# Kernel optimization log

Measured on AMD Instinct MI355X. Metric: run time of the kernel, lower is better.

## Reference

```python
import jax, jax.numpy as jnp
import numpy as np

# Module hyperparameters
P_, K_, NH = 8, 4, 8
B, H, W, C = 2, 64, 24, 256


def setup_inputs() -> dict:
    key = jax.random.key(0)
    ks = jax.random.split(key, 16)

    def w(k, shape, s=0.02):
        return (jax.random.normal(k, shape) * s).astype(jnp.float32)

    z = lambda *shape: jnp.zeros(shape, jnp.float32)
    return {
        'x_2d': jax.random.normal(ks[0], (B, H, W, C), dtype=jnp.float32),
        # block projections (used as x @ W + b)
        'wq_proj': w(ks[1], (C, C)), 'bq_proj': z(C),
        'wk_proj': w(ks[2], (C, C)), 'bk_proj': z(C),
        'wv_proj': w(ks[3], (C, C)), 'bv_proj': z(C),
        # routing attention projections
        'wq_a': w(ks[4], (C, C)), 'bq_a': z(C),
        'wk_a': w(ks[5], (C, C)), 'bk_a': z(C),
        'wv_a': w(ks[6], (C, C)), 'bv_a': z(C),
        'wo_a': w(ks[7], (C, C)), 'bo_a': z(C),
        # global conv path (HWIO, 5x5, SAME padding == torch padding=2)
        'conv_w': w(ks[8], (5, 5, C, C)), 'conv_b': z(C),
        # layer norms
        'ln1_g': jnp.ones((C,), jnp.float32), 'ln1_b': z(C),
        'ln2_g': jnp.ones((C,), jnp.float32), 'ln2_b': z(C),
    }


def _layer_norm(t, g, b, eps=1e-5):
    m = t.mean(-1, keepdims=True)
    v = ((t - m) ** 2).mean(-1, keepdims=True)
    return (t - m) / jnp.sqrt(v + eps) * g + b


def reference(x_2d, wq_proj, bq_proj, wk_proj, bk_proj, wv_proj, bv_proj,
              wq_a, bq_a, wk_a, bk_a, wv_a, bv_a, wo_a, bo_a,
              conv_w, conv_b, ln1_g, ln1_b, ln2_g, ln2_b):
    Bb, Hh, Ww, Cc = x_2d.shape
    hp = Hh // P_                      # block height
    dk = Cc // NH
    kv = min(K_, P_)

    x_p = x_2d.reshape(Bb, P_, hp, Ww, Cc)
    q_p = x_p @ wq_proj + bq_proj
    k_p = x_p @ wk_proj + bk_proj
    v_p = x_p @ wv_proj + bv_proj

    # block-level routing: mean-pooled block descriptors -> top-k blocks
    q_loc = q_p.mean((2, 3))           # [B,P,C]
    k_loc = k_p.mean((2, 3))
    S_loc = jnp.einsum('bpc,bqc->bpq', q_loc, k_loc)
    _, R = jax.lax.top_k(S_loc, kv)    # [B,P,kv] int32 indices into P

    # gather routed K/V blocks: [B,P,kv,hp*W,C]
    k_flat = k_p.reshape(Bb, P_, hp * Ww, Cc)
    v_flat = v_p.reshape(Bb, P_, hp * Ww, Cc)
    k_fil = jax.vmap(lambda t, r: t[r])(k_flat, R).reshape(Bb, P_, kv, hp, Ww, Cc)
    v_fil = jax.vmap(lambda t, r: t[r])(v_flat, R).reshape(Bb, P_, kv, hp, Ww, Cc)
    q_un = jnp.broadcast_to(q_p[:, :, None], (Bb, P_, kv, hp, Ww, Cc))

    # multi-head attention over flattened (kv*hp*W) per block p
    L = kv * hp * Ww
    def to_heads(t, w, b):
        t = t @ w + b
        t = t.reshape(Bb, P_, kv, hp, Ww, NH, dk)
        return t.transpose(0, 5, 1, 2, 3, 4, 6).reshape(Bb, NH, P_, L, dk)

    qh = to_heads(q_un, wq_a, bq_a)
    kh = to_heads(k_fil, wk_a, bk_a)
    vh = to_heads(v_fil, wv_a, bv_a)

    scores = jnp.einsum('bhpqd,bhpkd->bhpqk', qh, kh) / jnp.sqrt(jnp.float32(dk))
    attn = jax.nn.softmax(scores, axis=-1)
    ctx = jnp.einsum('bhpqk,bhpkd->bhpqd', attn, vh)
    # 'b h p (k hp w) dk -> b p k hp w (h dk)'
    ctx = ctx.reshape(Bb, NH, P_, kv, hp, Ww, dk).transpose(0, 2, 3, 4, 5, 1, 6)
    ctx = ctx.reshape(Bb, P_, kv, hp, Ww, Cc)
    routing_out = (ctx @ wo_a + bo_a).mean(2)          # [B,P,hp,W,C]

    x_res = _layer_norm(x_p + routing_out, ln1_g, ln1_b)

    # global conv path (NHWC SAME conv, kernel 5)
    kv_g = (k_p + v_p).reshape(Bb, Hh, Ww, Cc)
    g = jax.lax.conv_general_dilated(kv_g, conv_w, (1, 1), 'SAME',
                                     dimension_numbers=('NHWC', 'HWIO', 'NHWC')) + conv_b
    g = g.reshape(Bb, P_, hp, Ww, Cc)

    out = _layer_norm(x_res + g, ln2_g, ln2_b)
    return out.reshape(Bb, Hh, Ww, Cc)
```

## Files before the change

kernel.cpp:

```cpp
#include <hip/hip_runtime.h>
#include <hip/hip_bf16.h>


#define NPOS 3072
#define CD   256
#define NE   (NPOS*CD)

typedef short bf16x8 __attribute__((ext_vector_type(8)));
typedef float f32x4  __attribute__((ext_vector_type(4)));

__device__ inline ushort f2bf(float f) {
    __hip_bfloat16 h = __float2bfloat16(f);
    return *reinterpret_cast<ushort*>(&h);
}
__device__ inline float bf2f(ushort u) {
    unsigned v = ((unsigned)u) << 16;
    return *reinterpret_cast<float*>(&v);
}
__device__ inline bf16x8 addbf(bf16x8 a, bf16x8 b) {
    bf16x8 o;
    #pragma unroll
    for (int j = 0; j < 8; ++j)
        o[j] = (short)f2bf(bf2f((ushort)a[j]) + bf2f((ushort)b[j]));
    return o;
}

__global__ __launch_bounds__(256) void wtransA(
    const float* __restrict__ w0, const float* __restrict__ w1, const float* __restrict__ w2,
    const float* __restrict__ w3, const float* __restrict__ w4, const float* __restrict__ w5,
    const float* __restrict__ w6, const float* __restrict__ cw,
    ushort* __restrict__ wt, ushort* __restrict__ wct)
{
    __shared__ float l[64*65];
    int blk = blockIdx.x;
    const float* M;
    ushort* D;
    int r2;
    if (blk < 112) {
        int mat = blk >> 4; r2 = blk & 15;
        M = mat==0?w0:mat==1?w1:mat==2?w2:mat==3?w3:mat==4?w4:mat==5?w5:w6;
        D = wt + (size_t)mat*65536;
    } else {
        int b2 = blk - 112;
        int tap = b2 >> 4; r2 = b2 & 15;
        M = cw + (size_t)tap*65536;
        D = wct + (size_t)tap*65536;
    }
    int ci0 = (r2 >> 2)*64, co0 = (r2 & 3)*64;
    int tid = threadIdx.x, a = tid >> 6, c = tid & 63;
    #pragma unroll 4
    for (int k = 0; k < 16; ++k) {
        int cil = k*4 + a;
        l[cil*65 + c] = M[(size_t)(ci0 + cil)*256 + co0 + c];
    }
    __syncthreads();
    #pragma unroll 4
    for (int k = 0; k < 16; ++k) {
        int col = k*4 + a;
        D[((size_t)(co0 + col))*256 + ci0 + c] = f2bf(l[c*65 + col]);
    }
}

__global__ __launch_bounds__(256) void qkloc2(
    const float* __restrict__ x,
    const float* __restrict__ wq, const float* __restrict__ bq,
    const float* __restrict__ wk, const float* __restrict__ bk,
    float* __restrict__ qloc, float* __restrict__ kloc)
{
    __shared__ float xs[256];
    int bp = blockIdx.x, c = threadIdx.x;
    float s = 0.f;
    for (int i = 0; i < 192; ++i)
        s += x[((size_t)(bp*192 + i))*256 + c];
    xs[c] = s * (1.0f/192.0f);
    __syncthreads();
    const float* W  = blockIdx.y ? wk : wq;
    const float* Bv = blockIdx.y ? bk : bq;
    float* dst      = blockIdx.y ? kloc : qloc;
    float acc = Bv[c];
    #pragma unroll 8
    for (int k = 0; k < 256; ++k)
        acc += xs[k] * W[(size_t)k*256 + c];
    dst[bp*256 + c] = acc;
}

__global__ void topk_kern(const float* __restrict__ qloc, const float* __restrict__ kloc,
                          int* __restrict__ Rix)
{
    __shared__ float S[64];
    int b = blockIdx.x, t = threadIdx.x;
    int p = t >> 3, qq = t & 7;
    float s = 0.f;
    for (int c = 0; c < 256; ++c)
        s += qloc[(b*8+p)*256 + c] * kloc[(b*8+qq)*256 + c];
    S[t] = s;
    __syncthreads();
    if (t < 8) {
        float vals[8];
        #pragma unroll
        for (int j = 0; j < 8; ++j) vals[j] = S[t*8 + j];
        for (int j = 0; j < 4; ++j) {
            int best = 0; float bv = vals[0];
            #pragma unroll
            for (int i = 1; i < 8; ++i) if (vals[i] > bv) { bv = vals[i]; best = i; }
            Rix[(b*8 + t)*4 + j] = best;
            vals[best] = -1e30f;
        }
    }
}

__global__ __launch_bounds__(256) void gemm_btx3(
    const float* __restrict__ A,
    const ushort* __restrict__ T0, const ushort* __restrict__ T1, const ushort* __restrict__ T2,
    const float* __restrict__ B0, const float* __restrict__ B1, const float* __restrict__ B2,
    ushort* __restrict__ U0, ushort* __restrict__ U1, ushort* __restrict__ U2)
{
    __shared__ __align__(16) ushort As[32*264];
    int y = blockIdx.y;
    const ushort* T = y==0 ? T0 : (y==1 ? T1 : T2);
    const float* Bi = y==0 ? B0 : (y==1 ? B1 : B2);
    ushort* U = y==0 ? U0 : (y==1 ? U1 : U2);
    int tid = threadIdx.x;
    int m0 = (blockIdx.x >> 1)*32;
    int nh = blockIdx.x & 1;
    #pragma unroll
    for (int i = 0; i < 4; ++i) {
        int c = i*256 + tid;
        int pos = c >> 5, off = (c & 31)*8;
        const float* src = A + (size_t)(m0 + pos)*256 + off;
        float4 v0 = *(const float4*)src;
        float4 v1 = *(const float4*)(src + 4);
        ushort4 o0, o1;
        o0.x = f2bf(v0.x); o0.y = f2bf(v0.y); o0.z = f2bf(v0.z); o0.w = f2bf(v0.w);
        o1.x = f2bf(v1.x); o1.y = f2bf(v1.y); o1.z = f2bf(v1.z); o1.w = f2bf(v1.w);
        *(ushort4*)&As[pos*264 + off]     = o0;
        *(ushort4*)&As[pos*264 + off + 4] = o1;
    }
    __syncthreads();
    int w = tid >> 6, lane = tid & 63, lm = lane & 15, lq = lane >> 4;
    const ushort* tb = T + ((size_t)(nh*128 + w*32 + lm))*256 + lq*8;

    f32x4 acc[2][2];
    #pragma unroll
    for (int mt = 0; mt < 2; ++mt)
        #pragma unroll
        for (int nt = 0; nt < 2; ++nt) acc[mt][nt] = (f32x4){0.f,0.f,0.f,0.f};

    bf16x8 bw[2];
    #pragma unroll
    for (int nt = 0; nt < 2; ++nt) bw[nt] = *(const bf16x8*)(tb + nt*4096);

    for (int kc = 0; kc < 8; ++kc) {
        int nk = (kc + 1 < 8) ? kc + 1 : 7;
        bf16x8 bn[2];
        #pragma unroll
        for (int nt = 0; nt < 2; ++nt) bn[nt] = *(const bf16x8*)(tb + nt*4096 + nk*32);
        bf16x8 af[2];
        #pragma unroll
        for (int mt = 0; mt < 2; ++mt)
            af[mt] = *(const bf16x8*)&As[(mt*16 + lm)*264 + kc*32 + lq*8];
        #pragma unroll
        for (int mt = 0; mt < 2; ++mt)
            #pragma unroll
            for (int nt = 0; nt < 2; ++nt)
                acc[mt][nt] = __builtin_amdgcn_mfma_f32_16x16x32_bf16(af[mt], bw[nt], acc[mt][nt], 0,0,0);
        #pragma unroll
        for (int nt = 0; nt < 2; ++nt) bw[nt] = bn[nt];
    }

    #pragma unroll
    for (int mt = 0; mt < 2; ++mt) {
        #pragma unroll
        for (int nt = 0; nt < 2; ++nt) {
            int n = nh*128 + w*32 + nt*16 + lm;
            float bb = Bi[n];
            #pragma unroll
            for (int j = 0; j < 4; ++j) {
                int m = m0 + mt*16 + lq*4 + j;
                U[(size_t)m*256 + n] = f2bf(acc[mt][nt][j] + bb);
            }
        }
    }
}

__global__ __launch_bounds__(256) void gemm_bt3(
    const ushort* __restrict__ A0, const ushort* __restrict__ A1, const ushort* __restrict__ A2,
    const ushort* __restrict__ T0, const ushort* __restrict__ T1, const ushort* __restrict__ T2,
    const float* __restrict__ B0, const float* __restrict__ B1, const float* __restrict__ B2,
    ushort* __restrict__ U0, ushort* __restrict__ U1, ushort* __restrict__ U2,
    float s0, float s1, float s2)
{
    __shared__ __align__(16) ushort As[32*264];
    int y = blockIdx.y;
    const ushort* A = y==0 ? A0 : (y==1 ? A1 : A2);
    const ushort* T = y==0 ? T0 : (y==1 ? T1 : T2);
    const float* Bi = y==0 ? B0 : (y==1 ? B1 : B2);
    ushort* U = y==0 ? U0 : (y==1 ? U1 : U2);
    float  sc = y==0 ? s0 : (y==1 ? s1 : s2);
    int tid = threadIdx.x;
    int m0 = (blockIdx.x >> 1)*32;
    int nh = blockIdx.x & 1;
    #pragma unroll
    for (int i = 0; i < 4; ++i) {
        int c = i*256 + tid;
        int pos = c >> 5, off = (c & 31)*8;
        *(bf16x8*)&As[pos*264 + off] = *(const bf16x8*)(A + (size_t)(m0 + pos)*256 + off);
    }
    __syncthreads();
    int w = tid >> 6, lane = tid & 63, lm = lane & 15, lq = lane >> 4;
    const ushort* tb = T + ((size_t)(nh*128 + w*32 + lm))*256 + lq*8;

    f32x4 acc[2][2];
    #pragma unroll
    for (int mt = 0; mt < 2; ++mt)
        #pragma unroll
        for (int nt = 0; nt < 2; ++nt) acc[mt][nt] = (f32x4){0.f,0.f,0.f,0.f};

    bf16x8 bw[2];
    #pragma unroll
    for (int nt = 0; nt < 2; ++nt) bw[nt] = *(const bf16x8*)(tb + nt*4096);

    for (int kc = 0; kc < 8; ++kc) {
        int nk = (kc + 1 < 8) ? kc + 1 : 7;
        bf16x8 bn[2];
        #pragma unroll
        for (int nt = 0; nt < 2; ++nt) bn[nt] = *(const bf16x8*)(tb + nt*4096 + nk*32);
        bf16x8 af[2];
        #pragma unroll
        for (int mt = 0; mt < 2; ++mt)
            af[mt] = *(const bf16x8*)&As[(mt*16 + lm)*264 + kc*32 + lq*8];
        #pragma unroll
        for (int mt = 0; mt < 2; ++mt)
            #pragma unroll
            for (int nt = 0; nt < 2; ++nt)
                acc[mt][nt] = __builtin_amdgcn_mfma_f32_16x16x32_bf16(af[mt], bw[nt], acc[mt][nt], 0,0,0);
        #pragma unroll
        for (int nt = 0; nt < 2; ++nt) bw[nt] = bn[nt];
    }

    #pragma unroll
    for (int mt = 0; mt < 2; ++mt) {
        #pragma unroll
        for (int nt = 0; nt < 2; ++nt) {
            int n = nh*128 + w*32 + nt*16 + lm;
            float bb = Bi[n];
            #pragma unroll
            for (int j = 0; j < 4; ++j) {
                int m = m0 + mt*16 + lq*4 + j;
                U[(size_t)m*256 + n] = f2bf((acc[mt][nt][j] + bb) * sc);
            }
        }
    }
}

__global__ __launch_bounds__(256) void attn_mfma2(
    const ushort* __restrict__ qab, const ushort* __restrict__ kab,
    const ushort* __restrict__ vab, const int* __restrict__ Rix,
    float* __restrict__ pl, ushort* __restrict__ pacc)
{
    __shared__ ushort P[4][16*40];
    __shared__ ushort Vs[32*200];
    int tid = threadIdx.x, w = tid >> 6, lane = tid & 63;
    int lm = lane & 15, lq = lane >> 4;
    int bph = blockIdx.x, kvb = blockIdx.y;
    int bp = bph >> 3, h = bph & 7, b = bp >> 3;
    int r = Rix[bp*4 + kvb];
    int vrow0 = (b*8 + r)*192;

    #pragma unroll
    for (int i = 0; i < 6; ++i) {
        int idx = i*256 + tid;
        int pos = idx >> 3, c4 = (idx & 7)*4;
        ushort4 v = *(const ushort4*)(vab + ((size_t)(vrow0 + pos))*256 + h*32 + c4);
        Vs[(c4+0)*200 + pos] = v.x;
        Vs[(c4+1)*200 + pos] = v.y;
        Vs[(c4+2)*200 + pos] = v.z;
        Vs[(c4+3)*200 + pos] = v.w;
    }

    bf16x8 qf[3];
    #pragma unroll
    for (int t = 0; t < 3; ++t)
        qf[t] = *(const bf16x8*)(qab + ((size_t)(bp*192 + w*48 + t*16 + lm))*256 + h*32 + lq*8);

    const ushort* kbase = kab + ((size_t)(vrow0))*256 + h*32 + lq*8;
    ushort* pw = P[w];
    __syncthreads();

    f32x4 O[3][2];
    #pragma unroll
    for (int t = 0; t < 3; ++t) { O[t][0] = (f32x4){0,0,0,0}; O[t][1] = (f32x4){0,0,0,0}; }
    float l[3] = {0.f, 0.f, 0.f};

    for (int k0 = 0; k0 < 192; k0 += 32) {
        bf16x8 kf0 = *(const bf16x8*)(kbase + (size_t)(k0 + lm)*256);
        bf16x8 kf1 = *(const bf16x8*)(kbase + (size_t)(k0 + 16 + lm)*256);
        bf16x8 vf0 = *(const bf16x8*)(&Vs[lm*200 + k0 + lq*8]);
        bf16x8 vf1 = *(const bf16x8*)(&Vs[(16 + lm)*200 + k0 + lq*8]);
        #pragma unroll
        for (int t = 0; t < 3; ++t) {
            f32x4 s0 = __builtin_amdgcn_mfma_f32_16x16x32_bf16(kf0, qf[t], (f32x4){0,0,0,0}, 0,0,0);
            f32x4 s1 = __builtin_amdgcn_mfma_f32_16x16x32_bf16(kf1, qf[t], (f32x4){0,0,0,0}, 0,0,0);
            float p0[4], p1[4];
            #pragma unroll
            for (int j = 0; j < 4; ++j) { p0[j] = __expf(s0[j]); p1[j] = __expf(s1[j]); }
            l[t] += p0[0]+p0[1]+p0[2]+p0[3] + p1[0]+p1[1]+p1[2]+p1[3];
            ushort4 a, c;
            a.x = f2bf(p0[0]); a.y = f2bf(p0[1]); a.z = f2bf(p0[2]); a.w = f2bf(p0[3]);
            c.x = f2bf(p1[0]); c.y = f2bf(p1[1]); c.z = f2bf(p1[2]); c.w = f2bf(p1[3]);
            *(ushort4*)(pw + lm*40 + lq*4)      = a;
            *(ushort4*)(pw + lm*40 + 16 + lq*4) = c;
            bf16x8 pf = *(const bf16x8*)(pw + lm*40 + lq*8);
            O[t][0] = __builtin_amdgcn_mfma_f32_16x16x32_bf16(pf, vf0, O[t][0], 0,0,0);
            O[t][1] = __builtin_amdgcn_mfma_f32_16x16x32_bf16(pf, vf1, O[t][1], 0,0,0);
        }
    }

    #pragma unroll
    for (int t = 0; t < 3; ++t) {
        float lt = l[t];
        lt += __shfl_xor(lt, 16);
        lt += __shfl_xor(lt, 32);
        size_t pbase = ((size_t)(bph*4 + kvb))*192 + w*48 + t*16;
        if (lq == 0) pl[pbase + lm] = lt;
        #pragma unroll
        for (int nt = 0; nt < 2; ++nt)
            #pragma unroll
            for (int reg = 0; reg < 4; ++reg)
                pacc[(pbase + lq*4 + reg)*32 + nt*16 + lm] = f2bf(O[t][nt][reg]);
    }
}

__global__ __launch_bounds__(256) void gemm_wo_ln(
    const float* __restrict__ pl, const ushort* __restrict__ pacc,
    const ushort* __restrict__ T, const float* __restrict__ boa,
    const float* __restrict__ x,
    const float* __restrict__ g1, const float* __restrict__ b1,
    float* __restrict__ x_res)
{
    __shared__ __align__(16) ushort As[32*264];
    __shared__ float L2x[32*256];
    int tid = threadIdx.x;
    int m0 = blockIdx.x*32;
    #pragma unroll
    for (int i = 0; i < 4; ++i) {
        int c = i*256 + tid;
        int pos = c >> 5, off = (c & 31)*8;
        int m = m0 + pos;
        int bp = m / 192, q = m - bp*192;
        int h = off >> 5, d0 = off & 31;
        int bph = bp*8 + h;
        float ls = 0.f;
        float cv[8] = {0,0,0,0,0,0,0,0};
        #pragma unroll
        for (int k = 0; k < 4; ++k) {
            size_t pidx = ((size_t)(bph*4 + k))*192 + q;
            ls += pl[pidx];
            bf16x8 pv = *(const bf16x8*)(pacc + pidx*32 + d0);
            #pragma unroll
            for (int j = 0; j < 8; ++j) cv[j] += bf2f((ushort)pv[j]);
        }
        ushort o[8];
        #pragma unroll
        for (int j = 0; j < 8; ++j) o[j] = f2bf(cv[j] / ls);
        *(ushort4*)&As[pos*264 + off]     = make_ushort4(o[0],o[1],o[2],o[3]);
        *(ushort4*)&As[pos*264 + off + 4] = make_ushort4(o[4],o[5],o[6],o[7]);
    }
    __syncthreads();
    int w = tid >> 6, lane = tid & 63, lm = lane & 15, lq = lane >> 4;
    const ushort* tb = T + ((size_t)(w*64 + lm))*256 + lq*8;

    f32x4 acc[2][4];
    #pragma unroll
    for (int mt = 0; mt < 2; ++mt)
        #pragma unroll
        for (int nt = 0; nt < 4; ++nt) acc[mt][nt] = (f32x4){0.f,0.f,0.f,0.f};

    bf16x8 bw[4];
    #pragma unroll
    for (int nt = 0; nt < 4; ++nt) bw[nt] = *(const bf16x8*)(tb + nt*4096);

    for (int kc = 0; kc < 8; ++kc) {
        int nk = (kc + 1 < 8) ? kc + 1 : 7;
        bf16x8 bn[4];
        #pragma unroll
        for (int nt = 0; nt < 4; ++nt) bn[nt] = *(const bf16x8*)(tb + nt*4096 + nk*32);
        bf16x8 af[2];
        #pragma unroll
        for (int mt = 0; mt < 2; ++mt)
            af[mt] = *(const bf16x8*)&As[(mt*16 + lm)*264 + kc*32 + lq*8];
        #pragma unroll
        for (int mt = 0; mt < 2; ++mt)
            #pragma unroll
            for (int nt = 0; nt < 4; ++nt)
                acc[mt][nt] = __builtin_amdgcn_mfma_f32_16x16x32_bf16(af[mt], bw[nt], acc[mt][nt], 0,0,0);
        #pragma unroll
        for (int nt = 0; nt < 4; ++nt) bw[nt] = bn[nt];
    }

    #pragma unroll
    for (int mt = 0; mt < 2; ++mt) {
        #pragma unroll
        for (int nt = 0; nt < 4; ++nt) {
            int n = w*64 + nt*16 + lm;
            float bb = boa[n];
            #pragma unroll
            for (int j = 0; j < 4; ++j) {
                int pos = mt*16 + lq*4 + j;
                float val = acc[mt][nt][j] + bb;
                L2x[pos*256 + n] = val + x[(size_t)(m0 + pos)*256 + n];
            }
        }
    }
    __syncthreads();
    #pragma unroll
    for (int rr = 0; rr < 8; ++rr) {
        int pos = w*8 + rr;
        float4 a = *(const float4*)(&L2x[pos*256 + lane*4]);
        float x0 = a.x, x1 = a.y, x2 = a.z, x3 = a.w;
        float s  = x0 + x1 + x2 + x3;
        float sq = x0*x0 + x1*x1 + x2*x2 + x3*x3;
        #pragma unroll
        for (int off = 32; off > 0; off >>= 1) {
            s  += __shfl_xor(s,  off);
            sq += __shfl_xor(sq, off);
        }
        float mean = s * (1.0f/256.0f);
        float var  = sq * (1.0f/256.0f) - mean*mean;
        float rstd = rsqrtf(var + 1e-5f);
        float4 gv = *(const float4*)(g1 + lane*4);
        float4 bv = *(const float4*)(b1 + lane*4);
        float4 o;
        o.x = (x0 - mean)*rstd*gv.x + bv.x;
        o.y = (x1 - mean)*rstd*gv.y + bv.y;
        o.z = (x2 - mean)*rstd*gv.z + bv.z;
        o.w = (x3 - mean)*rstd*gv.w + bv.w;
        *(float4*)(x_res + (size_t)(m0 + pos)*256 + lane*4) = o;
    }
}

__global__ __launch_bounds__(256) void conv_mfma6(
    const ushort* __restrict__ kpb, const ushort* __restrict__ vpb,
    const ushort* __restrict__ wct, ushort* __restrict__ pconv)
{
    __shared__ __align__(16) ushort Arows[2][9504];
    int tid = threadIdx.x;
    int bid = blockIdx.x;
    int ch = bid & 1;
    int t2 = bid >> 1;
    int rp = t2 / 5, dy = t2 - rp*5;
    int b = rp >> 5, y0 = (rp & 31)*2;

    const bf16x8 zero8 = (bf16x8){0,0,0,0,0,0,0,0};
    #pragma unroll
    for (int i = 0; i < 7; ++i) {
        int c = i*256 + tid;
        int row = (c >= 896);
        int cc = c - row*896;
        int pos = cc >> 5, off = (cc & 31)*8;
        int y = y0 + row + dy - 2;
        bf16x8 v = zero8;
        if (y >= 0 && y < 64 && pos >= 2 && pos < 26) {
            size_t sb = ((size_t)((b*64 + y)*24 + (pos - 2)))*256 + off;
            v = addbf(*(const bf16x8*)(kpb + sb), *(const bf16x8*)(vpb + sb));
        }
        *(bf16x8*)(&Arows[row][pos*264 + off]) = v;
    }
    __syncthreads();

    int w = tid >> 6;
    int lane = tid & 63, lm = lane & 15, lq = lane >> 4;
    const ushort* bbase = wct + ((size_t)((dy*5)*256 + ch*128 + w*32 + lm))*256 + lq*8;
    const ushort* a00 = &Arows[0][lm*264 + lq*8];

    f32x4 acc[2][2][2];
    #pragma unroll
    for (int r = 0; r < 2; ++r)
        #pragma unroll
        for (int mt = 0; mt < 2; ++mt)
            #pragma unroll
            for (int nt = 0; nt < 2; ++nt)
                acc[r][mt][nt] = (f32x4){0.f,0.f,0.f,0.f};

    bf16x8 b0[2], b1[2];
    #pragma unroll
    for (int nt = 0; nt < 2; ++nt) b0[nt] = *(const bf16x8*)(bbase + nt*4096);
    #pragma unroll
    for (int nt = 0; nt < 2; ++nt) b1[nt] = *(const bf16x8*)(bbase + 32 + nt*4096);

    for (int iter = 0; iter < 40; ++iter) {
        int i2 = (iter + 2 < 40) ? iter + 2 : 39;
        int boff = (i2 >> 3)*65536 + (i2 & 7)*32;
        bf16x8 bn[2];
        #pragma unroll
        for (int nt = 0; nt < 2; ++nt) bn[nt] = *(const bf16x8*)(bbase + boff + nt*4096);

        int aoff = (iter >> 3)*264 + (iter & 7)*32;
        bf16x8 af[2][2];
        #pragma unroll
        for (int r = 0; r < 2; ++r)
            #pragma unroll
            for (int mt = 0; mt < 2; ++mt)
                af[r][mt] = *(const bf16x8*)(a00 + r*9504 + mt*4224 + aoff);

        #pragma unroll
        for (int r = 0; r < 2; ++r)
            #pragma unroll
            for (int mt = 0; mt < 2; ++mt)
                #pragma unroll
                for (int nt = 0; nt < 2; ++nt)
                    acc[r][mt][nt] = __builtin_amdgcn_mfma_f32_16x16x32_bf16(
                        af[r][mt], b0[nt], acc[r][mt][nt], 0, 0, 0);

        #pragma unroll
        for (int nt = 0; nt < 2; ++nt) { b0[nt] = b1[nt]; b1[nt] = bn[nt]; }
    }

    #pragma unroll
    for (int r = 0; r < 2; ++r) {
        int grow = rp*2 + r;
        #pragma unroll
        for (int mt = 0; mt < 2; ++mt) {
            #pragma unroll
            for (int nt = 0; nt < 2; ++nt) {
                int cob = ch*128 + w*32 + nt*16 + lm;
                #pragma unroll
                for (int j = 0; j < 4; ++j) {
                    int x = mt*16 + lq*4 + j;
                    if (x < 24)
                        pconv[((size_t)(dy*3072 + grow*24 + x))*256 + cob]
                            = f2bf(acc[r][mt][nt][j]);
                }
            }
        }
    }
}

__global__ __launch_bounds__(256) void ln2_fused(
    const float* __restrict__ xr, const ushort* __restrict__ pc, const float* __restrict__ cb,
    const float* __restrict__ gamma, const float* __restrict__ beta,
    float* __restrict__ out)
{
    int pos  = blockIdx.x*4 + (threadIdx.x >> 6);
    int lane = threadIdx.x & 63;
    size_t base = (size_t)pos*256 + lane*4;
    float4 gsum = *(const float4*)(cb + lane*4);
    #pragma unroll
    for (int d = 0; d < 5; ++d) {
        ushort4 v = *(const ushort4*)(pc + (size_t)d*NE + base);
        gsum.x += bf2f(v.x); gsum.y += bf2f(v.y);
        gsum.z += bf2f(v.z); gsum.w += bf2f(v.w);
    }
    float4 a = *(const float4*)(xr + base);
    float x0 = a.x + gsum.x, x1 = a.y + gsum.y, x2 = a.z + gsum.z, x3 = a.w + gsum.w;
    float s  = x0 + x1 + x2 + x3;
    float sq = x0*x0 + x1*x1 + x2*x2 + x3*x3;
    #pragma unroll
    for (int off = 32; off > 0; off >>= 1) {
        s  += __shfl_xor(s,  off);
        sq += __shfl_xor(sq, off);
    }
    float mean = s * (1.0f/256.0f);
    float var  = sq * (1.0f/256.0f) - mean*mean;
    float rstd = rsqrtf(var + 1e-5f);
    float4 gv = *(const float4*)(gamma + lane*4);
    float4 bv = *(const float4*)(beta  + lane*4);
    float4 o;
    o.x = (x0 - mean)*rstd*gv.x + bv.x;
    o.y = (x1 - mean)*rstd*gv.y + bv.y;
    o.z = (x2 - mean)*rstd*gv.z + bv.z;
    o.w = (x3 - mean)*rstd*gv.w + bv.w;
    *(float4*)(out + base) = o;
}

extern "C" void kernel_launch(void* const* d_in, const int* in_sizes, int n_in,
                              void* d_out, int out_size, void* d_ws, size_t ws_size,
                              hipStream_t stream)
{
    (void)in_sizes; (void)n_in; (void)out_size; (void)ws_size;
    const float* x    = (const float*)d_in[0];
    const float* wq   = (const float*)d_in[1];
    const float* bq   = (const float*)d_in[2];
    const float* wk   = (const float*)d_in[3];
    const float* bk   = (const float*)d_in[4];
    const float* wv   = (const float*)d_in[5];
    const float* bv   = (const float*)d_in[6];
    const float* wqa  = (const float*)d_in[7];
    const float* bqa  = (const float*)d_in[8];
    const float* wka  = (const float*)d_in[9];
    const float* bka  = (const float*)d_in[10];
    const float* wva  = (const float*)d_in[11];
    const float* bva  = (const float*)d_in[12];
    const float* woa  = (const float*)d_in[13];
    const float* boa  = (const float*)d_in[14];
    const float* cw   = (const float*)d_in[15];
    const float* cbi  = (const float*)d_in[16];
    const float* ln1g = (const float*)d_in[17];
    const float* ln1b = (const float*)d_in[18];
    const float* ln2g = (const float*)d_in[19];
    const float* ln2b = (const float*)d_in[20];
    float* out = (float*)d_out;

    float* ws = (float*)d_ws;
    const size_t HNE = NE/2;
    ushort* qpb = (ushort*)(ws + 0*HNE);
    ushort* kpb = (ushort*)(ws + 1*HNE);
    ushort* vpb = (ushort*)(ws + 3*HNE);
    ushort* qab = (ushort*)(ws + 4*HNE);
    ushort* kab = (ushort*)(ws + 5*HNE);
    ushort* vab = (ushort*)(ws + 6*HNE);
    float* x_res = (float*)(ws + 6*HNE);
    float* R    = ws + 8*HNE;
    ushort* pacc = (ushort*)R;
    float*  pl   = R + 1572864;
    ushort* pconv= (ushort*)R;
    ushort* wt7 = (ushort*)(R + 3932160);
    ushort* wct = (ushort*)(R + 3932160 + 229376);
    float* qloc = R + 3932160 + 229376 + 819200;
    float* kloc = qloc + 4096;
    int*   Rix  = (int*)(kloc + 4096);

    wtransA<<<512, 256, 0, stream>>>(wq,wk,wv,wqa,wka,wva,woa, cw, wt7, wct);
    qkloc2<<<dim3(16,2), 256, 0, stream>>>(x, wq,bq, wk,bk, qloc, kloc);
    topk_kern<<<2, 64, 0, stream>>>(qloc, kloc, Rix);
    gemm_btx3<<<dim3(192,3), 256, 0, stream>>>(
        x, wt7, wt7+65536, wt7+131072, bq,bk,bv, qpb,kpb,vpb);
    gemm_bt3<<<dim3(192,3), 256, 0, stream>>>(
        qpb,kpb,vpb, wt7+196608, wt7+262144, wt7+327680, bqa,bka,bva,
        qab,kab,vab, 0.17677669529663687f,1.f,1.f);
    attn_mfma2<<<dim3(128,4), 256, 0, stream>>>(qab, kab, vab, Rix, pl, pacc);
    gemm_wo_ln<<<96, 256, 0, stream>>>(pl, pacc, wt7+393216, boa, x, ln1g, ln1b, x_res);
    conv_mfma6<<<640, 256, 0, stream>>>(kpb, vpb, wct, pconv);
    ln2_fused<<<NPOS/4, 256, 0, stream>>>(x_res, pconv, cbi, ln2g, ln2b, out);
}
```

Measured before the change: 206.2 us.

## Merge independent kernels into shared launches and fuse LN2 into Wo GEMM epilogue

Combines the weight transpose and block-descriptor projection into one launch using block-index dispatch, and runs the conv and the attention in a single launch so the two independent workloads share the GPU. The second layer norm (conv-partial reduction plus LN) moves into the Wo GEMM epilogue, which removes the x_res round trip through memory and two kernel launches. The conv output buffer is relocated so it no longer aliases the attention partials. The shared-memory footprint of the merged kernel grows to the conv's size for the attention blocks, which may lower their occupancy.

```diff
diff --git a/kernel.cpp b/kernel.cpp
--- a/kernel.cpp
+++ b/kernel.cpp
@@ -25,63 +25,64 @@
     return o;
 }
 
-__global__ __launch_bounds__(256) void wtransA(
+__global__ __launch_bounds__(256) void wtrans_qkloc(
     const float* __restrict__ w0, const float* __restrict__ w1, const float* __restrict__ w2,
     const float* __restrict__ w3, const float* __restrict__ w4, const float* __restrict__ w5,
     const float* __restrict__ w6, const float* __restrict__ cw,
-    ushort* __restrict__ wt, ushort* __restrict__ wct)
-{
-    __shared__ float l[64*65];
-    int blk = blockIdx.x;
-    const float* M;
-    ushort* D;
-    int r2;
-    if (blk < 112) {
-        int mat = blk >> 4; r2 = blk & 15;
-        M = mat==0?w0:mat==1?w1:mat==2?w2:mat==3?w3:mat==4?w4:mat==5?w5:w6;
-        D = wt + (size_t)mat*65536;
-    } else {
-        int b2 = blk - 112;
-        int tap = b2 >> 4; r2 = b2 & 15;
-        M = cw + (size_t)tap*65536;
-        D = wct + (size_t)tap*65536;
-    }
-    int ci0 = (r2 >> 2)*64, co0 = (r2 & 3)*64;
-    int tid = threadIdx.x, a = tid >> 6, c = tid & 63;
-    #pragma unroll 4
-    for (int k = 0; k < 16; ++k) {
-        int cil = k*4 + a;
-        l[cil*65 + c] = M[(size_t)(ci0 + cil)*256 + co0 + c];
-    }
-    __syncthreads();
-    #pragma unroll 4
-    for (int k = 0; k < 16; ++k) {
-        int col = k*4 + a;
-        D[((size_t)(co0 + col))*256 + ci0 + c] = f2bf(l[c*65 + col]);
-    }
-}
-
-__global__ __launch_bounds__(256) void qkloc2(
+    ushort* __restrict__ wt, ushort* __restrict__ wct,
     const float* __restrict__ x,
     const float* __restrict__ wq, const float* __restrict__ bq,
     const float* __restrict__ wk, const float* __restrict__ bk,
     float* __restrict__ qloc, float* __restrict__ kloc)
 {
-    __shared__ float xs[256];
-    int bp = blockIdx.x, c = threadIdx.x;
-    float s = 0.f;
-    for (int i = 0; i < 192; ++i)
-        s += x[((size_t)(bp*192 + i))*256 + c];
-    xs[c] = s * (1.0f/192.0f);
-    __syncthreads();
-    const float* W  = blockIdx.y ? wk : wq;
-    const float* Bv = blockIdx.y ? bk : bq;
-    float* dst      = blockIdx.y ? kloc : qloc;
-    float acc = Bv[c];
-    #pragma unroll 8
-    for (int k = 0; k < 256; ++k)
-        acc += xs[k] * W[(size_t)k*256 + c];
-    dst[bp*256 + c] = acc;
+    __shared__ float l[64*65];
+    int blk = blockIdx.x;
+    int tid = threadIdx.x;
+    if (blk < 512) {
+        const float* M;
+        ushort* D;
+        int r2;
+        if (blk < 112) {
+            int mat = blk >> 4; r2 = blk & 15;
+            M = mat==0?w0:mat==1?w1:mat==2?w2:mat==3?w3:mat==4?w4:mat==5?w5:w6;
+            D = wt + (size_t)mat*65536;
+        } else {
+            int b2 = blk - 112;
+            int tap = b2 >> 4; r2 = b2 & 15;
+            M = cw + (size_t)tap*65536;
+            D = wct + (size_t)tap*65536;
+        }
+        int ci0 = (r2 >> 2)*64, co0 = (r2 & 3)*64;
+        int a = tid >> 6, c = tid & 63;
+        #pragma unroll 4
+        for (int k = 0; k < 16; ++k) {
+            int cil = k*4 + a;
+            l[cil*65 + c] = M[(size_t)(ci0 + cil)*256 + co0 + c];
+        }
+        __syncthreads();
+        #pragma unroll 4
+        for (int k = 0; k < 16; ++k) {
+            int col = k*4 + a;
+            D[((size_t)(co0 + col))*256 + ci0 + c] = f2bf(l[c*65 + col]);
+        }
+    } else {
+        int q2 = blk - 512;
+        int bp = q2 & 15, which = q2 >> 4;
+        int c = tid;
+        float s = 0.f;
+        for (int i = 0; i < 192; ++i)
+            s += x[((size_t)(bp*192 + i))*256 + c];
+        l[c] = s * (1.0f/192.0f);
+        __syncthreads();
+        const float* W  = which ? wk : wq;
+        const float* Bv = which ? bk : bq;
+        float* dst      = which ? kloc : qloc;
+        float acc = Bv[c];
+        #pragma unroll 8
+        for (int k = 0; k < 256; ++k)
+            acc += l[k] * W[(size_t)k*256 + c];
+        dst[bp*256 + c] = acc;
+    }
 }
 
 __global__ void topk_kern(const float* __restrict__ qloc, const float* __restrict__ kloc,
@@ -253,90 +254,189 @@
     }
 }
 
-__global__ __launch_bounds__(256) void attn_mfma2(
+__global__ __launch_bounds__(256) void attn_conv(
     const ushort* __restrict__ qab, const ushort* __restrict__ kab,
     const ushort* __restrict__ vab, const int* __restrict__ Rix,
-    float* __restrict__ pl, ushort* __restrict__ pacc)
+    float* __restrict__ pl, ushort* __restrict__ pacc,
+    const ushort* __restrict__ kpb, const ushort* __restrict__ vpb,
+    const ushort* __restrict__ wct, ushort* __restrict__ pconv)
 {
-    __shared__ ushort P[4][16*40];
-    __shared__ ushort Vs[32*200];
-    int tid = threadIdx.x, w = tid >> 6, lane = tid & 63;
-    int lm = lane & 15, lq = lane >> 4;
-    int bph = blockIdx.x, kvb = blockIdx.y;
-    int bp = bph >> 3, h = bph & 7, b = bp >> 3;
-    int r = Rix[bp*4 + kvb];
-    int vrow0 = (b*8 + r)*192;
-
-    #pragma unroll
-    for (int i = 0; i < 6; ++i) {
-        int idx = i*256 + tid;
-        int pos = idx >> 3, c4 = (idx & 7)*4;
-        ushort4 v = *(const ushort4*)(vab + ((size_t)(vrow0 + pos))*256 + h*32 + c4);
-        Vs[(c4+0)*200 + pos] = v.x;
-        Vs[(c4+1)*200 + pos] = v.y;
-        Vs[(c4+2)*200 + pos] = v.z;
-        Vs[(c4+3)*200 + pos] = v.w;
-    }
-
-    bf16x8 qf[3];
-    #pragma unroll
-    for (int t = 0; t < 3; ++t)
-        qf[t] = *(const bf16x8*)(qab + ((size_t)(bp*192 + w*48 + t*16 + lm))*256 + h*32 + lq*8);
-
-    const ushort* kbase = kab + ((size_t)(vrow0))*256 + h*32 + lq*8;
-    ushort* pw = P[w];
-    __syncthreads();
-
-    f32x4 O[3][2];
-    #pragma unroll
-    for (int t = 0; t < 3; ++t) { O[t][0] = (f32x4){0,0,0,0}; O[t][1] = (f32x4){0,0,0,0}; }
-    float l[3] = {0.f, 0.f, 0.f};
-
-    for (int k0 = 0; k0 < 192; k0 += 32) {
-        bf16x8 kf0 = *(const bf16x8*)(kbase + (size_t)(k0 + lm)*256);
-        bf16x8 kf1 = *(const bf16x8*)(kbase + (size_t)(k0 + 16 + lm)*256);
-        bf16x8 vf0 = *(const bf16x8*)(&Vs[lm*200 + k0 + lq*8]);
-        bf16x8 vf1 = *(const bf16x8*)(&Vs[(16 + lm)*200 + k0 + lq*8]);
+    __shared__ __align__(16) ushort SMEM[19008];
+    int tid = threadIdx.x;
+    int bid = blockIdx.x;
+    if (bid < 640) {
+        int ch = bid & 1;
+        int t2 = bid >> 1;
+        int rp = t2 / 5, dy = t2 - rp*5;
+        int b = rp >> 5, y0 = (rp & 31)*2;
+
+        const bf16x8 zero8 = (bf16x8){0,0,0,0,0,0,0,0};
+        #pragma unroll
+        for (int i = 0; i < 7; ++i) {
+            int c = i*256 + tid;
+            int row = (c >= 896);
+            int cc = c - row*896;
+            int pos = cc >> 5, off = (cc & 31)*8;
+            int y = y0 + row + dy - 2;
+            bf16x8 v = zero8;
+            if (y >= 0 && y < 64 && pos >= 2 && pos < 26) {
+                size_t sb = ((size_t)((b*64 + y)*24 + (pos - 2)))*256 + off;
+                v = addbf(*(const bf16x8*)(kpb + sb), *(const bf16x8*)(vpb + sb));
+            }
+            *(bf16x8*)(&SMEM[row*9504 + pos*264 + off]) = v;
+        }
+        __syncthreads();
+
+        int w = tid >> 6;
+        int lane = tid & 63, lm = lane & 15, lq = lane >> 4;
+        const ushort* bbase = wct + ((size_t)((dy*5)*256 + ch*128 + w*32 + lm))*256 + lq*8;
+        const ushort* a00 = &SMEM[lm*264 + lq*8];
+
+        f32x4 acc[2][2][2];
+        #pragma unroll
+        for (int r = 0; r < 2; ++r)
+            #pragma unroll
+            for (int mt = 0; mt < 2; ++mt)
+                #pragma unroll
+                for (int nt = 0; nt < 2; ++nt)
+                    acc[r][mt][nt] = (f32x4){0.f,0.f,0.f,0.f};
+
+        bf16x8 b0[2], b1[2];
+        #pragma unroll
+        for (int nt = 0; nt < 2; ++nt) b0[nt] = *(const bf16x8*)(bbase + nt*4096);
+        #pragma unroll
+        for (int nt = 0; nt < 2; ++nt) b1[nt] = *(const bf16x8*)(bbase + 32 + nt*4096);
+
+        for (int iter = 0; iter < 40; ++iter) {
+            int i2 = (iter + 2 < 40) ? iter + 2 : 39;
+            int boff = (i2 >> 3)*65536 + (i2 & 7)*32;
+            bf16x8 bn[2];
+            #pragma unroll
+            for (int nt = 0; nt < 2; ++nt) bn[nt] = *(const bf16x8*)(bbase + boff + nt*4096);
+
+            int aoff = (iter >> 3)*264 + (iter & 7)*32;
+            bf16x8 af[2][2];
+            #pragma unroll
+            for (int r = 0; r < 2; ++r)
+                #pragma unroll
+                for (int mt = 0; mt < 2; ++mt)
+                    af[r][mt] = *(const bf16x8*)(a00 + r*9504 + mt*4224 + aoff);
+
+            #pragma unroll
+            for (int r = 0; r < 2; ++r)
+                #pragma unroll
+                for (int mt = 0; mt < 2; ++mt)
+                    #pragma unroll
+                    for (int nt = 0; nt < 2; ++nt)
+                        acc[r][mt][nt] = __builtin_amdgcn_mfma_f32_16x16x32_bf16(
+                            af[r][mt], b0[nt], acc[r][mt][nt], 0, 0, 0);
+
+            #pragma unroll
+            for (int nt = 0; nt < 2; ++nt) { b0[nt] = b1[nt]; b1[nt] = bn[nt]; }
+        }
+
+        #pragma unroll
+        for (int r = 0; r < 2; ++r) {
+            int grow = rp*2 + r;
+            #pragma unroll
+            for (int mt = 0; mt < 2; ++mt) {
+                #pragma unroll
+                for (int nt = 0; nt < 2; ++nt) {
+                    int cob = ch*128 + w*32 + nt*16 + lm;
+                    #pragma unroll
+                    for (int j = 0; j < 4; ++j) {
+                        int x = mt*16 + lq*4 + j;
+                        if (x < 24)
+                            pconv[((size_t)(dy*3072 + grow*24 + x))*256 + cob]
+                                = f2bf(acc[r][mt][nt][j]);
+                    }
+                }
+            }
+        }
+    } else {
+        int id = bid - 640;
+        int bph = id >> 2, kvb = id & 3;
+        int w = tid >> 6, lane = tid & 63;
+        int lm = lane & 15, lq = lane >> 4;
+        int bp = bph >> 3, h = bph & 7, b = bp >> 3;
+        int r = Rix[bp*4 + kvb];
+        int vrow0 = (b*8 + r)*192;
+        ushort* P  = SMEM;
+        ushort* Vs = SMEM + 2560;
+
+        #pragma unroll
+        for (int i = 0; i < 6; ++i) {
+            int idx = i*256 + tid;
+            int pos = idx >> 3, c4 = (idx & 7)*4;
+            ushort4 v = *(const ushort4*)(vab + ((size_t)(vrow0 + pos))*256 + h*32 + c4);
+            Vs[(c4+0)*200 + pos] = v.x;
+            Vs[(c4+1)*200 + pos] = v.y;
+            Vs[(c4+2)*200 + pos] = v.z;
+            Vs[(c4+3)*200 + pos] = v.w;
+        }
+
+        bf16x8 qf[3];
+        #pragma unroll
+        for (int t = 0; t < 3; ++t)
+            qf[t] = *(const bf16x8*)(qab + ((size_t)(bp*192 + w*48 + t*16 + lm))*256 + h*32 + lq*8);
+
+        const ushort* kbase = kab + ((size_t)(vrow0))*256 + h*32 + lq*8;
+        ushort* pw = P + w*640;
+        __syncthreads();
+
+        f32x4 O[3][2];
+        #pragma unroll
+        for (int t = 0; t < 3; ++t) { O[t][0] = (f32x4){0,0,0,0}; O[t][1] = (f32x4){0,0,0,0}; }
+        float l[3] = {0.f, 0.f, 0.f};
+
+        for (int k0 = 0; k0 < 192; k0 += 32) {
+            bf16x8 kf0 = *(const bf16x8*)(kbase + (size_t)(k0 + lm)*256);
+            bf16x8 kf1 = *(const bf16x8*)(kbase + (size_t)(k0 + 16 + lm)*256);
+            bf16x8 vf0 = *(const bf16x8*)(&Vs[lm*200 + k0 + lq*8]);
+            bf16x8 vf1 = *(const bf16x8*)(&Vs[(16 + lm)*200 + k0 + lq*8]);
+            #pragma unroll
+            for (int t = 0; t < 3; ++t) {
+                f32x4 s0 = __builtin_amdgcn_mfma_f32_16x16x32_bf16(kf0, qf[t], (f32x4){0,0,0,0}, 0,0,0);
+                f32x4 s1 = __builtin_amdgcn_mfma_f32_16x16x32_bf16(kf1, qf[t], (f32x4){0,0,0,0}, 0,0,0);
+                float p0[4], p1[4];
+                #pragma unroll
+                for (int j = 0; j < 4; ++j) { p0[j] = __expf(s0[j]); p1[j] = __expf(s1[j]); }
+                l[t] += p0[0]+p0[1]+p0[2]+p0[3] + p1[0]+p1[1]+p1[2]+p1[3];
+                ushort4 a, c;
+                a.x = f2bf(p0[0]); a.y = f2bf(p0[1]); a.z = f2bf(p0[2]); a.w = f2bf(p0[3]);
+                c.x = f2bf(p1[0]); c.y = f2bf(p1[1]); c.z = f2bf(p1[2]); c.w = f2bf(p1[3]);
+                *(ushort4*)(pw + lm*40 + lq*4)      = a;
+                *(ushort4*)(pw + lm*40 + 16 + lq*4) = c;
+                bf16x8 pf = *(const bf16x8*)(pw + lm*40 + lq*8);
+                O[t][0] = __builtin_amdgcn_mfma_f32_16x16x32_bf16(pf, vf0, O[t][0], 0,0,0);
+                O[t][1] = __builtin_amdgcn_mfma_f32_16x16x32_bf16(pf, vf1, O[t][1], 0,0,0);
+            }
+        }
+
         #pragma unroll
         for (int t = 0; t < 3; ++t) {
-            f32x4 s0 = __builtin_amdgcn_mfma_f32_16x16x32_bf16(kf0, qf[t], (f32x4){0,0,0,0}, 0,0,0);
-            f32x4 s1 = __builtin_amdgcn_mfma_f32_16x16x32_bf16(kf1, qf[t], (f32x4){0,0,0,0}, 0,0,0);
-            float p0[4], p1[4];
-            #pragma unroll
-            for (int j = 0; j < 4; ++j) { p0[j] = __expf(s0[j]); p1[j] = __expf(s1[j]); }
-            l[t] += p0[0]+p0[1]+p0[2]+p0[3] + p1[0]+p1[1]+p1[2]+p1[3];
-            ushort4 a, c;
-            a.x = f2bf(p0[0]); a.y = f2bf(p0[1]); a.z = f2bf(p0[2]); a.w = f2bf(p0[3]);
-            c.x = f2bf(p1[0]); c.y = f2bf(p1[1]); c.z = f2bf(p1[2]); c.w = f2bf(p1[3]);
-            *(ushort4*)(pw + lm*40 + lq*4)      = a;
-            *(ushort4*)(pw + lm*40 + 16 + lq*4) = c;
-            bf16x8 pf = *(const bf16x8*)(pw + lm*40 + lq*8);
-            O[t][0] = __builtin_amdgcn_mfma_f32_16x16x32_bf16(pf, vf0, O[t][0], 0,0,0);
-            O[t][1] = __builtin_amdgcn_mfma_f32_16x16x32_bf16(pf, vf1, O[t][1], 0,0,0);
-        }
-    }
-
-    #pragma unroll
-    for (int t = 0; t < 3; ++t) {
-        float lt = l[t];
-        lt += __shfl_xor(lt, 16);
-        lt += __shfl_xor(lt, 32);
-        size_t pbase = ((size_t)(bph*4 + kvb))*192 + w*48 + t*16;
-        if (lq == 0) pl[pbase + lm] = lt;
-        #pragma unroll
-        for (int nt = 0; nt < 2; ++nt)
-            #pragma unroll
-            for (int reg = 0; reg < 4; ++reg)
-                pacc[(pbase + lq*4 + reg)*32 + nt*16 + lm] = f2bf(O[t][nt][reg]);
-    }
-}
-
-__global__ __launch_bounds__(256) void gemm_wo_ln(
+            float lt = l[t];
+            lt += __shfl_xor(lt, 16);
+            lt += __shfl_xor(lt, 32);
+            size_t pbase = ((size_t)(bph*4 + kvb))*192 + w*48 + t*16;
+            if (lq == 0) pl[pbase + lm] = lt;
+            #pragma unroll
+            for (int nt = 0; nt < 2; ++nt)
+                #pragma unroll
+                for (int reg = 0; reg < 4; ++reg)
+                    pacc[(pbase + lq*4 + reg)*32 + nt*16 + lm] = f2bf(O[t][nt][reg]);
+        }
+    }
+}
+
+__global__ __launch_bounds__(256) void gemm_wo_ln2(
     const float* __restrict__ pl, const ushort* __restrict__ pacc,
     const ushort* __restrict__ T, const float* __restrict__ boa,
     const float* __restrict__ x,
     const float* __restrict__ g1, const float* __restrict__ b1,
-    float* __restrict__ x_res)
+    const ushort* __restrict__ pc, const float* __restrict__ cb,
+    const float* __restrict__ g2, const float* __restrict__ b2,
+    float* __restrict__ out)
 {
     __shared__ __align__(16) ushort As[32*264];
     __shared__ float L2x[32*256];
@@ -416,6 +516,7 @@
     #pragma unroll
     for (int rr = 0; rr < 8; ++rr) {
         int pos = w*8 + rr;
+        int grow = m0 + pos;
         float4 a = *(const float4*)(&L2x[pos*256 + lane*4]);
         float x0 = a.x, x1 = a.y, x2 = a.z, x3 = a.w;
         float s  = x0 + x1 + x2 + x3;
@@ -430,147 +531,38 @@
         float rstd = rsqrtf(var + 1e-5f);
         float4 gv = *(const float4*)(g1 + lane*4);
         float4 bv = *(const float4*)(b1 + lane*4);
+        float r0 = (x0 - mean)*rstd*gv.x + bv.x;
+        float r1 = (x1 - mean)*rstd*gv.y + bv.y;
+        float r2 = (x2 - mean)*rstd*gv.z + bv.z;
+        float r3 = (x3 - mean)*rstd*gv.w + bv.w;
+        size_t base = (size_t)grow*256 + lane*4;
+        float4 gsum = *(const float4*)(cb + lane*4);
+        #pragma unroll
+        for (int d = 0; d < 5; ++d) {
+            ushort4 v = *(const ushort4*)(pc + (size_t)d*NE + base);
+            gsum.x += bf2f(v.x); gsum.y += bf2f(v.y);
+            gsum.z += bf2f(v.z); gsum.w += bf2f(v.w);
+        }
+        float y0 = r0 + gsum.x, y1 = r1 + gsum.y, y2 = r2 + gsum.z, y3 = r3 + gsum.w;
+        float s2v  = y0 + y1 + y2 + y3;
+        float sq2  = y0*y0 + y1*y1 + y2*y2 + y3*y3;
+        #pragma unroll
+        for (int off = 32; off > 0; off >>= 1) {
+            s2v += __shfl_xor(s2v, off);
+            sq2 += __shfl_xor(sq2, off);
+        }
+        float mean2 = s2v * (1.0f/256.0f);
+        float var2  = sq2 * (1.0f/256.0f) - mean2*mean2;
+        float rstd2 = rsqrtf(var2 + 1e-5f);
+        float4 g2v = *(const float4*)(g2 + lane*4);
+        float4 b2v = *(const float4*)(b2 + lane*4);
         float4 o;
-        o.x = (x0 - mean)*rstd*gv.x + bv.x;
-        o.y = (x1 - mean)*rstd*gv.y + bv.y;
-        o.z = (x2 - mean)*rstd*gv.z + bv.z;
-        o.w = (x3 - mean)*rstd*gv.w + bv.w;
-        *(float4*)(x_res + (size_t)(m0 + pos)*256 + lane*4) = o;
-    }
-}
-
-__global__ __launch_bounds__(256) void conv_mfma6(
-    const ushort* __restrict__ kpb, const ushort* __restrict__ vpb,
-    const ushort* __restrict__ wct, ushort* __restrict__ pconv)
-{
-    __shared__ __align__(16) ushort Arows[2][9504];
-    int tid = threadIdx.x;
-    int bid = blockIdx.x;
-    int ch = bid & 1;
-    int t2 = bid >> 1;
-    int rp = t2 / 5, dy = t2 - rp*5;
-    int b = rp >> 5, y0 = (rp & 31)*2;
-
-    const bf16x8 zero8 = (bf16x8){0,0,0,0,0,0,0,0};
-    #pragma unroll
-    for (int i = 0; i < 7; ++i) {
-        int c = i*256 + tid;
-        int row = (c >= 896);
-        int cc = c - row*896;
-        int pos = cc >> 5, off = (cc & 31)*8;
-        int y = y0 + row + dy - 2;
-        bf16x8 v = zero8;
-        if (y >= 0 && y < 64 && pos >= 2 && pos < 26) {
-            size_t sb = ((size_t)((b*64 + y)*24 + (pos - 2)))*256 + off;
-            v = addbf(*(const bf16x8*)(kpb + sb), *(const bf16x8*)(vpb + sb));
-        }
-        *(bf16x8*)(&Arows[row][pos*264 + off]) = v;
-    }
-    __syncthreads();
-
-    int w = tid >> 6;
-    int lane = tid & 63, lm = lane & 15, lq = lane >> 4;
-    const ushort* bbase = wct + ((size_t)((dy*5)*256 + ch*128 + w*32 + lm))*256 + lq*8;
-    const ushort* a00 = &Arows[0][lm*264 + lq*8];
-
-    f32x4 acc[2][2][2];
-    #pragma unroll
-    for (int r = 0; r < 2; ++r)
-        #pragma unroll
-        for (int mt = 0; mt < 2; ++mt)
-            #pragma unroll
-            for (int nt = 0; nt < 2; ++nt)
-                acc[r][mt][nt] = (f32x4){0.f,0.f,0.f,0.f};
-
-    bf16x8 b0[2], b1[2];
-    #pragma unroll
-    for (int nt = 0; nt < 2; ++nt) b0[nt] = *(const bf16x8*)(bbase + nt*4096);
-    #pragma unroll
-    for (int nt = 0; nt < 2; ++nt) b1[nt] = *(const bf16x8*)(bbase + 32 + nt*4096);
-
-    for (int iter = 0; iter < 40; ++iter) {
-        int i2 = (iter + 2 < 40) ? iter + 2 : 39;
-        int boff = (i2 >> 3)*65536 + (i2 & 7)*32;
-        bf16x8 bn[2];
-        #pragma unroll
-        for (int nt = 0; nt < 2; ++nt) bn[nt] = *(const bf16x8*)(bbase + boff + nt*4096);
-
-        int aoff = (iter >> 3)*264 + (iter & 7)*32;
-        bf16x8 af[2][2];
-        #pragma unroll
-        for (int r = 0; r < 2; ++r)
-            #pragma unroll
-            for (int mt = 0; mt < 2; ++mt)
-                af[r][mt] = *(const bf16x8*)(a00 + r*9504 + mt*4224 + aoff);
-
-        #pragma unroll
-        for (int r = 0; r < 2; ++r)
-            #pragma unroll
-            for (int mt = 0; mt < 2; ++mt)
-                #pragma unroll
-                for (int nt = 0; nt < 2; ++nt)
-                    acc[r][mt][nt] = __builtin_amdgcn_mfma_f32_16x16x32_bf16(
-                        af[r][mt], b0[nt], acc[r][mt][nt], 0, 0, 0);
-
-        #pragma unroll
-        for (int nt = 0; nt < 2; ++nt) { b0[nt] = b1[nt]; b1[nt] = bn[nt]; }
-    }
-
-    #pragma unroll
-    for (int r = 0; r < 2; ++r) {
-        int grow = rp*2 + r;
-        #pragma unroll
-        for (int mt = 0; mt < 2; ++mt) {
-            #pragma unroll
-            for (int nt = 0; nt < 2; ++nt) {
-                int cob = ch*128 + w*32 + nt*16 + lm;
-                #pragma unroll
-                for (int j = 0; j < 4; ++j) {
-                    int x = mt*16 + lq*4 + j;
-                    if (x < 24)
-                        pconv[((size_t)(dy*3072 + grow*24 + x))*256 + cob]
-                            = f2bf(acc[r][mt][nt][j]);
-                }
-            }
-        }
-    }
-}
-
-__global__ __launch_bounds__(256) void ln2_fused(
-    const float* __restrict__ xr, const ushort* __restrict__ pc, const float* __restrict__ cb,
-    const float* __restrict__ gamma, const float* __restrict__ beta,
-    float* __restrict__ out)
-{
-    int pos  = blockIdx.x*4 + (threadIdx.x >> 6);
-    int lane = threadIdx.x & 63;
-    size_t base = (size_t)pos*256 + lane*4;
-    float4 gsum = *(const float4*)(cb + lane*4);
-    #pragma unroll
-    for (int d = 0; d < 5; ++d) {
-        ushort4 v = *(const ushort4*)(pc + (size_t)d*NE + base);
-        gsum.x += bf2f(v.x); gsum.y += bf2f(v.y);
-        gsum.z += bf2f(v.z); gsum.w += bf2f(v.w);
-    }
-    float4 a = *(const float4*)(xr + base);
-    float x0 = a.x + gsum.x, x1 = a.y + gsum.y, x2 = a.z + gsum.z, x3 = a.w + gsum.w;
-    float s  = x0 + x1 + x2 + x3;
-    float sq = x0*x0 + x1*x1 + x2*x2 + x3*x3;
-    #pragma unroll
-    for (int off = 32; off > 0; off >>= 1) {
-        s  += __shfl_xor(s,  off);
-        sq += __shfl_xor(sq, off);
-    }
-    float mean = s * (1.0f/256.0f);
-    float var  = sq * (1.0f/256.0f) - mean*mean;
-    float rstd = rsqrtf(var + 1e-5f);
-    float4 gv = *(const float4*)(gamma + lane*4);
-    float4 bv = *(const float4*)(beta  + lane*4);
-    float4 o;
-    o.x = (x0 - mean)*rstd*gv.x + bv.x;
-    o.y = (x1 - mean)*rstd*gv.y + bv.y;
-    o.z = (x2 - mean)*rstd*gv.z + bv.z;
-    o.w = (x3 - mean)*rstd*gv.w + bv.w;
-    *(float4*)(out + base) = o;
+        o.x = (y0 - mean2)*rstd2*g2v.x + b2v.x;
+        o.y = (y1 - mean2)*rstd2*g2v.y + b2v.y;
+        o.z = (y2 - mean2)*rstd2*g2v.z + b2v.z;
+        o.w = (y3 - mean2)*rstd2*g2v.w + b2v.w;
+        *(float4*)(out + base) = o;
+    }
 }
 
 extern "C" void kernel_launch(void* const* d_in, const int* in_sizes, int n_in,
@@ -609,27 +601,26 @@
     ushort* qab = (ushort*)(ws + 4*HNE);
     ushort* kab = (ushort*)(ws + 5*HNE);
     ushort* vab = (ushort*)(ws + 6*HNE);
-    float* x_res = (float*)(ws + 6*HNE);
     float* R    = ws + 8*HNE;
     ushort* pacc = (ushort*)R;
     float*  pl   = R + 1572864;
-    ushort* pconv= (ushort*)R;
+    ushort* pconv= (ushort*)(R + 1671168);
     ushort* wt7 = (ushort*)(R + 3932160);
     ushort* wct = (ushort*)(R + 3932160 + 229376);
     float* qloc = R + 3932160 + 229376 + 819200;
     float* kloc = qloc + 4096;
     int*   Rix  = (int*)(kloc + 4096);
 
-    wtransA<<<512, 256, 0, stream>>>(wq,wk,wv,wqa,wka,wva,woa, cw, wt7, wct);
-    qkloc2<<<dim3(16,2), 256, 0, stream>>>(x, wq,bq, wk,bk, qloc, kloc);
+    wtrans_qkloc<<<544, 256, 0, stream>>>(wq,wk,wv,wqa,wka,wva,woa, cw, wt7, wct,
+                                          x, wq,bq, wk,bk, qloc, kloc);
     topk_kern<<<2, 64, 0, stream>>>(qloc, kloc, Rix);
     gemm_btx3<<<dim3(192,3), 256, 0, stream>>>(
         x, wt7, wt7+65536, wt7+131072, bq,bk,bv, qpb,kpb,vpb);
     gemm_bt3<<<dim3(192,3), 256, 0, stream>>>(
         qpb,kpb,vpb, wt7+196608, wt7+262144, wt7+327680, bqa,bka,bva,
         qab,kab,vab, 0.17677669529663687f,1.f,1.f);
-    attn_mfma2<<<dim3(128,4), 256, 0, stream>>>(qab, kab, vab, Rix, pl, pacc);
-    gemm_wo_ln<<<96, 256, 0, stream>>>(pl, pacc, wt7+393216, boa, x, ln1g, ln1b, x_res);
-    conv_mfma6<<<640, 256, 0, stream>>>(kpb, vpb, wct, pconv);
-    ln2_fused<<<NPOS/4, 256, 0, stream>>>(x_res, pconv, cbi, ln2g, ln2b, out);
-}
+    attn_conv<<<1152, 256, 0, stream>>>(qab, kab, vab, Rix, pl, pacc,
+                                        kpb, vpb, wct, pconv);
+    gemm_wo_ln2<<<96, 256, 0, stream>>>(pl, pacc, wt7+393216, boa, x, ln1g, ln1b,
+                                        pconv, cbi, ln2g, ln2b, out);
+}
```

Result: no change. 203.9 us (-1.1%).
